# Kernel optimization log

Measured on AMD Instinct MI355X. Metric: run time of the kernel, lower is better.

The kernel has to match this reference:

```python
import jax, jax.numpy as jnp
import numpy as np

B, S, H = 1, 4096, 2048
NH, HD = 16, 128  # num_heads, head_dim = H // NH


def setup_inputs() -> dict:
    key = jax.random.key(0)
    k1, k2, k3 = jax.random.split(key, 3)
    x = jax.random.normal(k1, (B, S, H), dtype=jnp.float32)
    w_qkv = jax.random.normal(k2, (3 * H, H), dtype=jnp.float32) * (1.0 / np.sqrt(H))
    w_out = jax.random.normal(k3, (H, H), dtype=jnp.float32) * (1.0 / np.sqrt(H))
    return {"x": x, "w_qkv": w_qkv, "w_out": w_out}


def reference(x, w_qkv, w_out):
    b, s, _ = x.shape
    # qkv projection: torch Linear computes x @ W^T
    qkv = jnp.einsum('bsh,oh->bso', x, w_qkv)
    qkv = qkv.reshape(b, s, 3, NH, HD).transpose(2, 0, 3, 1, 4)  # [3,B,NH,S,HD]
    q, k, v = qkv[0], qkv[1], qkv[2]
    # world_size == 1 -> single ring step == full attention with online softmax
    scores = jnp.einsum('bhqd,bhkd->bhqk', q, k) / np.sqrt(HD)
    m = jnp.max(scores, axis=-1, keepdims=True)          # running max (single step)
    p = jnp.exp(scores - m)                              # scores_exp
    out = jnp.einsum('bhqk,bhkd->bhqd', p, v)
    denom = jnp.sum(p, axis=-1, keepdims=True) + 1e-8    # running_sum + eps
    out = out / denom
    out = out.transpose(0, 2, 1, 3).reshape(b, s, H)     # [B,S,H]
    return jnp.einsum('bsh,oh->bso', out, w_out)
```

## Files before the change

### kernel.cpp

```cpp
#include <hip/hip_runtime.h>
#include <stdint.h>

typedef __attribute__((ext_vector_type(4))) float f32x4;
typedef __attribute__((ext_vector_type(16))) float f32x16;
typedef __attribute__((ext_vector_type(8))) short bf16x8;
typedef unsigned short u16;

#define MFMA(a, b, c) __builtin_amdgcn_mfma_f32_16x16x32_bf16(a, b, c, 0, 0, 0)
#define MFMA32(a, b, c) __builtin_amdgcn_mfma_f32_32x32x16_bf16(a, b, c, 0, 0, 0)
#define EXP2(x) __builtin_amdgcn_exp2f(x)

__device__ __forceinline__ u16 f2bf(float f) {
  union { float f; unsigned u; } x; x.f = f;
  unsigned r = x.u + 0x7fffu + ((x.u >> 16) & 1u);
  return (u16)(r >> 16);
}

__device__ __forceinline__ unsigned cvtpk(float lo, float hi) {
  unsigned r;
  asm("v_cvt_pk_bf16_f32 %0, %1, %2" : "=v"(r) : "v"(lo), "v"(hi));
  return r;
}

__device__ __forceinline__ void pl32swap(unsigned& a, unsigned& b) {
  asm volatile("v_permlane32_swap_b32 %0, %1" : "+v"(a), "+v"(b));
}

__device__ __forceinline__ void gload16(const void* g, void* l) {
  __builtin_amdgcn_global_load_lds(
      (const __attribute__((address_space(1))) unsigned int*)g,
      (__attribute__((address_space(3))) unsigned int*)l, 16, 0, 0);
}

__global__ void __launch_bounds__(256) cast_bf16(const float* __restrict__ in,
                                                 u16* __restrict__ out, int n4) {
  int i = blockIdx.x * 256 + threadIdx.x;
  if (i >= n4) return;
  float4 v = reinterpret_cast<const float4*>(in)[i];
  ushort4 o;
  o.x = f2bf(v.x); o.y = f2bf(v.y); o.z = f2bf(v.z); o.w = f2bf(v.w);
  reinterpret_cast<ushort4*>(out)[i] = o;
}

template <int EPI>
__global__ void __launch_bounds__(256, 2)
gemm_bt(const u16* __restrict__ A, const u16* __restrict__ B,
        void* __restrict__ C0, void* __restrict__ C1, void* __restrict__ C2,
        int M, int N, int K, int MB) {
  __shared__ alignas(16) u16 sm[8192];
  const int tid = threadIdx.x;
  const int w = tid >> 6, lane = tid & 63;
  const int lr = lane & 15, g = lane >> 4;
  const int gb = (blockIdx.x & 7) * ((int)gridDim.x >> 3) + (blockIdx.x >> 3);
  const int mb = gb % MB, nb = gb / MB;
  const int m0 = mb * 128, n0 = nb * 128;

  const u16* src[4];
  u16* dst[4];
#pragma unroll
  for (int i = 0; i < 4; ++i) {
    int c = w * 4 + i;
    int r = (c & 7) * 16 + (lane >> 2);
    int sb = (lane & 3) ^ ((r >> 1) & 3);
    src[i] = (c < 8) ? (A + (size_t)(m0 + r) * K + sb * 8)
                     : (B + (size_t)(n0 + r) * K + sb * 8);
    dst[i] = &sm[c * 512];
  }

  f32x4 acc[4][4];
#pragma unroll
  for (int x = 0; x < 4; ++x)
#pragma unroll
    for (int y = 0; y < 4; ++y) acc[x][y] = f32x4{0.f, 0.f, 0.f, 0.f};

  const int rowb = (w >> 1) * 64, colb = (w & 1) * 64;
  const int nk = K >> 5;
  for (int kt = 0; kt < nk; ++kt) {
#pragma unroll
    for (int i = 0; i < 4; ++i) gload16(src[i] + kt * 32, dst[i]);
    __syncthreads();
    bf16x8 af[4], bfr[4];
#pragma unroll
    for (int mi = 0; mi < 4; ++mi) {
      int r = rowb + mi * 16 + lr;
      af[mi] = *(const bf16x8*)((const char*)sm + r * 64 +
                                ((g * 16) ^ (((r >> 1) & 3) << 4)));
    }
#pragma unroll
    for (int ni = 0; ni < 4; ++ni) {
      int r = colb + ni * 16 + lr;
      bfr[ni] = *(const bf16x8*)((const char*)sm + 8192 + r * 64 +
                                 ((g * 16) ^ (((r >> 1) & 3) << 4)));
    }
#pragma unroll
    for (int mi = 0; mi < 4; ++mi)
#pragma unroll
      for (int ni = 0; ni < 4; ++ni)
        acc[mi][ni] = MFMA(af[mi], bfr[ni], acc[mi][ni]);
    __syncthreads();
  }

  if (EPI == 0) {
    u16* qo = (u16*)C0;
    u16* ko = (u16*)C1;
    u16* vo = (u16*)C2;
#pragma unroll
    for (int mi = 0; mi < 4; ++mi) {
      int s0 = m0 + rowb + mi * 16 + g * 4;
#pragma unroll
      for (int ni = 0; ni < 4; ++ni) {
        int n = n0 + colb + ni * 16 + lr;
        int t = n >> 11, hh = (n >> 7) & 15, d = n & 127;
        if (t == 2) {
          ushort4 pk;
          pk.x = f2bf(acc[mi][ni][0]);
          pk.y = f2bf(acc[mi][ni][1]);
          pk.z = f2bf(acc[mi][ni][2]);
          pk.w = f2bf(acc[mi][ni][3]);
          *(ushort4*)(vo + (size_t)(hh * 128 + d) * 4096 + s0) = pk;
        } else {
          u16* dq = (t == 0 ? qo : ko) + (size_t)(hh * 4096 + s0) * 128 + d;
#pragma unroll
          for (int j = 0; j < 4; ++j) dq[(size_t)j * 128] = f2bf(acc[mi][ni][j]);
        }
      }
    }
  } else {
    float* C = (float*)C0;
#pragma unroll
    for (int mi = 0; mi < 4; ++mi)
#pragma unroll
      for (int ni = 0; ni < 4; ++ni) {
        size_t r0 = (size_t)(m0 + rowb + mi * 16 + g * 4);
        int cn = n0 + colb + ni * 16 + lr;
#pragma unroll
        for (int j = 0; j < 4; ++j) C[(r0 + j) * N + cn] = acc[mi][ni][j];
      }
  }
}

__global__ void __launch_bounds__(256, 2)
attn_kernel(const u16* __restrict__ qg, const u16* __restrict__ kg,
            const u16* __restrict__ vtg, u16* __restrict__ og) {
  __shared__ alignas(16) u16 sm[32768];
  const int tid = threadIdx.x;
  const int w = tid >> 6, lane = tid & 63;
  const int ql = lane & 31, hl = lane >> 5;
  const int gb = (blockIdx.x & 7) * 64 + (blockIdx.x >> 3);
  const int h = gb >> 5;
  const int qb = gb & 31;

  const u16* ssrc[8];
  u16* sdst[8];
  size_t sstep;
  if (w < 2) {
    sstep = 64 * 128;
#pragma unroll
    for (int i = 0; i < 8; ++i) {
      int c = (w & 1) * 8 + i;
      int r = c * 4 + (lane >> 4);
      int sb = (lane & 15) ^ (r & 7);
      ssrc[i] = kg + (size_t)(h * 4096 + r) * 128 + sb * 8;
      sdst[i] = &sm[c * 512];
    }
  } else {
    sstep = 64;
#pragma unroll
    for (int i = 0; i < 8; ++i) {
      int c = (w & 1) * 8 + i;
      int r = c * 8 + (lane >> 3);
      int sb = (lane & 7) ^ (r & 7);
      ssrc[i] = vtg + (size_t)(h * 128 + r) * 4096 + sb * 8;
      sdst[i] = &sm[16384 + c * 512];
    }
  }

  const u16* qrow = qg + (size_t)(h * 4096 + qb * 128 + w * 32 + ql) * 128 + hl * 8;
  bf16x8 qf[8];
#pragma unroll
  for (int s = 0; s < 8; ++s) qf[s] = *(const bf16x8*)(qrow + s * 16);

  f32x16 of[4];
#pragma unroll
  for (int i = 0; i < 4; ++i)
#pragma unroll
    for (int r = 0; r < 16; ++r) of[i][r] = 0.f;
  float mrun = -1e30f, lsum = 0.f;
  const float sc2 = 0.08838834764831845f * 1.4426950408889634f;
  const float thr = 6.0f / sc2;

#pragma unroll
  for (int i = 0; i < 8; ++i) gload16(ssrc[i], sdst[i]);

  for (int t = 0; t < 64; ++t) {
    const int cur = t & 1;
    asm volatile("s_waitcnt vmcnt(0)" ::: "memory");
    __builtin_amdgcn_s_barrier();
    asm volatile("" ::: "memory");
    if (t + 1 < 64) {
      const int nb = (t + 1) & 1;
#pragma unroll
      for (int i = 0; i < 8; ++i)
        gload16(ssrc[i] + (size_t)(t + 1) * sstep, sdst[i] + nb * 8192);
    }
    const char* kbuf = (const char*)sm + cur * 16384;
    const char* vbuf = (const char*)sm + 32768 + cur * 16384;

    f32x16 st0, st1;
#pragma unroll
    for (int r = 0; r < 16; ++r) { st0[r] = 0.f; st1[r] = 0.f; }
    const int swz = (ql & 7) << 4;
    __builtin_amdgcn_s_setprio(1);
#pragma unroll
    for (int s = 0; s < 8; ++s) {
      int off = (s * 32 + hl * 16) ^ swz;
      bf16x8 k0 = *(const bf16x8*)(kbuf + ql * 256 + off);
      bf16x8 k1 = *(const bf16x8*)(kbuf + (32 + ql) * 256 + off);
      st0 = MFMA32(k0, qf[s], st0);
      st1 = MFMA32(k1, qf[s], st1);
    }
    __builtin_amdgcn_s_setprio(0);

    float tmax = -1e30f;
#pragma unroll
    for (int r = 0; r < 16; ++r) tmax = fmaxf(tmax, fmaxf(st0[r], st1[r]));
    tmax = fmaxf(tmax, __shfl_xor(tmax, 32));
    if (!__all(tmax - mrun <= thr)) {
      float mnew = fmaxf(mrun, tmax);
      float esc = EXP2((mrun - mnew) * sc2);
#pragma unroll
      for (int db = 0; db < 4; ++db)
#pragma unroll
        for (int r = 0; r < 16; ++r) of[db][r] *= esc;
      lsum *= esc;
      mrun = mnew;
    }
    float mb2 = mrun * sc2;
    float psum = 0.f;
    unsigned pk0[8], pk1[8];
#pragma unroll
    for (int i = 0; i < 8; ++i) {
      float a0 = EXP2(st0[2 * i] * sc2 - mb2);
      float b0 = EXP2(st0[2 * i + 1] * sc2 - mb2);
      float a1 = EXP2(st1[2 * i] * sc2 - mb2);
      float b1 = EXP2(st1[2 * i + 1] * sc2 - mb2);
      psum += (a0 + b0) + (a1 + b1);
      pk0[i] = cvtpk(a0, b0);
      pk1[i] = cvtpk(a1, b1);
    }
    psum += __shfl_xor(psum, 32);
    lsum += psum;

    pl32swap(pk0[0], pk0[2]); pl32swap(pk0[1], pk0[3]);
    pl32swap(pk0[4], pk0[6]); pl32swap(pk0[5], pk0[7]);
    pl32swap(pk1[0], pk1[2]); pl32swap(pk1[1], pk1[3]);
    pl32swap(pk1[4], pk1[6]); pl32swap(pk1[5], pk1[7]);
    union U { unsigned u[4]; bf16x8 v; };
    U paf[4];
#pragma unroll
    for (int i = 0; i < 4; ++i) { paf[0].u[i] = pk0[i]; paf[1].u[i] = pk0[4 + i]; }
#pragma unroll
    for (int i = 0; i < 4; ++i) { paf[2].u[i] = pk1[i]; paf[3].u[i] = pk1[4 + i]; }

    __builtin_amdgcn_s_setprio(1);
#pragma unroll
    for (int db = 0; db < 4; ++db) {
      int rr = db * 32 + ql;
      int vswz = (rr & 7) << 4;
#pragma unroll
      for (int kp = 0; kp < 4; ++kp) {
        bf16x8 vf = *(const bf16x8*)(vbuf + rr * 128 + ((kp * 32 + hl * 16) ^ vswz));
        of[db] = MFMA32(vf, paf[kp].v, of[db]);
      }
    }
    __builtin_amdgcn_s_setprio(0);
    asm volatile("" ::: "memory");
  }

  float linv = 1.f / (lsum + 1e-8f);
  size_t qrow_o = (size_t)(qb * 128 + w * 32 + ql) * 2048 + h * 128;
#pragma unroll
  for (int db = 0; db < 4; ++db)
#pragma unroll
    for (int u = 0; u < 4; ++u) {
      ushort4 pk;
      pk.x = f2bf(of[db][4 * u + 0] * linv);
      pk.y = f2bf(of[db][4 * u + 1] * linv);
      pk.z = f2bf(of[db][4 * u + 2] * linv);
      pk.w = f2bf(of[db][4 * u + 3] * linv);
      *(ushort4*)(og + qrow_o + db * 32 + 8 * u + hl * 4) = pk;
    }
}

extern "C" void kernel_launch(void* const* d_in, const int* in_sizes, int n_in,
                              void* d_out, int out_size, void* d_ws, size_t ws_size,
                              hipStream_t stream) {
  const float* x = (const float*)d_in[0];
  const float* w_qkv = (const float*)d_in[1];
  const float* w_out = (const float*)d_in[2];

  char* ws = (char*)d_ws;
  u16* xb = (u16*)(ws + 0);
  u16* wqkvb = (u16*)(ws + 16777216);
  u16* woutb = (u16*)(ws + 41943040);
  u16* qb = (u16*)(ws + 50331648);
  u16* kb = (u16*)(ws + 67108864);
  u16* vtb = (u16*)(ws + 83886080);
  u16* aob = (u16*)(ws + 100663296);

  cast_bf16<<<8192, 256, 0, stream>>>(x, xb, 2097152);
  cast_bf16<<<12288, 256, 0, stream>>>(w_qkv, wqkvb, 3145728);
  cast_bf16<<<4096, 256, 0, stream>>>(w_out, woutb, 1048576);

  gemm_bt<0><<<32 * 48, 256, 0, stream>>>(xb, wqkvb, qb, kb, vtb, 4096, 6144, 2048, 32);
  attn_kernel<<<512, 256, 0, stream>>>(qb, kb, vtb, aob);
  gemm_bt<1><<<32 * 16, 256, 0, stream>>>(aob, woutb, d_out, nullptr, nullptr, 4096, 2048, 2048, 32);
}
```

Measured before the change: 360.5 us.

## Load V fragments directly from global into registers, stage only K in LDS

The attention kernel stops staging the V^T tile in shared memory. Each wave now loads its V fragments straight from global memory into registers at the start of each iteration, and only K is double-buffered in LDS. This halves LDS usage and drops the LDS reads for V. The K swizzle widens to 16 lanes, and vmcnt waits are tuned to overlap the V loads with the QK^T and softmax phase. The trade-offs are higher register pressure (64 extra VGPRs for V) and redundant global V reads across the four waves, which now rely on the cache. The prefetch also wraps around and issues a useless final K load.

Result: slower. 457.0 us (+26.8%).

```diff
diff --git a/kernel.cpp b/kernel.cpp
--- a/kernel.cpp
+++ b/kernel.cpp
@@ -142,7 +142,7 @@
 __global__ void __launch_bounds__(256, 2)
 attn_kernel(const u16* __restrict__ qg, const u16* __restrict__ kg,
             const u16* __restrict__ vtg, u16* __restrict__ og) {
-  __shared__ alignas(16) u16 sm[32768];
+  __shared__ alignas(16) u16 sm[16384];
   const int tid = threadIdx.x;
   const int w = tid >> 6, lane = tid & 63;
   const int ql = lane & 31, hl = lane >> 5;
@@ -150,30 +150,21 @@
   const int h = gb >> 5;
   const int qb = gb & 31;
 
-  const u16* ssrc[8];
-  u16* sdst[8];
-  size_t sstep;
-  if (w < 2) {
-    sstep = 64 * 128;
-#pragma unroll
-    for (int i = 0; i < 8; ++i) {
-      int c = (w & 1) * 8 + i;
-      int r = c * 4 + (lane >> 4);
-      int sb = (lane & 15) ^ (r & 7);
-      ssrc[i] = kg + (size_t)(h * 4096 + r) * 128 + sb * 8;
-      sdst[i] = &sm[c * 512];
-    }
-  } else {
-    sstep = 64;
-#pragma unroll
-    for (int i = 0; i < 8; ++i) {
-      int c = (w & 1) * 8 + i;
-      int r = c * 8 + (lane >> 3);
-      int sb = (lane & 7) ^ (r & 7);
-      ssrc[i] = vtg + (size_t)(h * 128 + r) * 4096 + sb * 8;
-      sdst[i] = &sm[16384 + c * 512];
-    }
-  }
+  const u16* ssrc[4];
+  u16* sdst[4];
+#pragma unroll
+  for (int i = 0; i < 4; ++i) {
+    int c = w * 4 + i;
+    int r = c * 4 + (lane >> 4);
+    int sb = (lane & 15) ^ (r & 15);
+    ssrc[i] = kg + (size_t)(h * 4096 + r) * 128 + sb * 8;
+    sdst[i] = &sm[c * 512];
+  }
+
+  const u16* vbase[4];
+#pragma unroll
+  for (int db = 0; db < 4; ++db)
+    vbase[db] = vtg + (size_t)(h * 128 + db * 32 + ql) * 4096 + hl * 8;
 
   const u16* qrow = qg + (size_t)(h * 4096 + qb * 128 + w * 32 + ql) * 128 + hl * 8;
   bf16x8 qf[8];
@@ -190,30 +181,38 @@
   const float thr = 6.0f / sc2;
 
 #pragma unroll
-  for (int i = 0; i < 8; ++i) gload16(ssrc[i], sdst[i]);
-
+  for (int i = 0; i < 4; ++i) gload16(ssrc[i], sdst[i]);
+
+  const int kxor = (ql & 15) << 4;
   for (int t = 0; t < 64; ++t) {
     const int cur = t & 1;
-    asm volatile("s_waitcnt vmcnt(0)" ::: "memory");
+
+    bf16x8 vfr[4][4];
+#pragma unroll
+    for (int db = 0; db < 4; ++db)
+#pragma unroll
+      for (int kp = 0; kp < 4; ++kp)
+        vfr[db][kp] = *(const bf16x8*)(vbase[db] + t * 64 + kp * 16);
+
+    asm volatile("s_waitcnt vmcnt(16)" ::: "memory");
     __builtin_amdgcn_s_barrier();
-    asm volatile("" ::: "memory");
-    if (t + 1 < 64) {
-      const int nb = (t + 1) & 1;
-#pragma unroll
-      for (int i = 0; i < 8; ++i)
-        gload16(ssrc[i] + (size_t)(t + 1) * sstep, sdst[i] + nb * 8192);
+
+    {
+      const int tn = (t + 1) & 63;
+      const int nb = cur ^ 1;
+#pragma unroll
+      for (int i = 0; i < 4; ++i)
+        gload16(ssrc[i] + (size_t)tn * 8192, sdst[i] + nb * 8192);
     }
     const char* kbuf = (const char*)sm + cur * 16384;
-    const char* vbuf = (const char*)sm + 32768 + cur * 16384;
 
     f32x16 st0, st1;
 #pragma unroll
     for (int r = 0; r < 16; ++r) { st0[r] = 0.f; st1[r] = 0.f; }
-    const int swz = (ql & 7) << 4;
     __builtin_amdgcn_s_setprio(1);
 #pragma unroll
     for (int s = 0; s < 8; ++s) {
-      int off = (s * 32 + hl * 16) ^ swz;
+      int off = ((s * 2 + hl) << 4) ^ kxor;
       bf16x8 k0 = *(const bf16x8*)(kbuf + ql * 256 + off);
       bf16x8 k1 = *(const bf16x8*)(kbuf + (32 + ql) * 256 + off);
       st0 = MFMA32(k0, qf[s], st0);
@@ -262,19 +261,15 @@
 #pragma unroll
     for (int i = 0; i < 4; ++i) { paf[2].u[i] = pk1[i]; paf[3].u[i] = pk1[4 + i]; }
 
+    asm volatile("s_waitcnt vmcnt(4)" ::: "memory");
+
     __builtin_amdgcn_s_setprio(1);
 #pragma unroll
-    for (int db = 0; db < 4; ++db) {
-      int rr = db * 32 + ql;
-      int vswz = (rr & 7) << 4;
-#pragma unroll
-      for (int kp = 0; kp < 4; ++kp) {
-        bf16x8 vf = *(const bf16x8*)(vbuf + rr * 128 + ((kp * 32 + hl * 16) ^ vswz));
-        of[db] = MFMA32(vf, paf[kp].v, of[db]);
-      }
-    }
+    for (int db = 0; db < 4; ++db)
+#pragma unroll
+      for (int kp = 0; kp < 4; ++kp)
+        of[db] = MFMA32(vfr[db][kp], paf[kp].v, of[db]);
     __builtin_amdgcn_s_setprio(0);
-    asm volatile("" ::: "memory");
   }
 
   float linv = 1.f / (lsum + 1e-8f);
```

## Fold softmax scale into Q projection and widen LDS swizzle for K/V tiles

Applied to the files above, without the earlier changes.

The QKV projection epilogue now multiplies Q by the softmax scale times log2(e) before converting to bf16. This lets the attention loop compute exp2(s - m) directly and drops a multiply per score element. The K and V shared-memory layouts switch to a 16-way XOR swizzle, with V pairing two rows per 256-byte line, to reduce LDS bank conflicts on the MFMA operand reads. Pre-scaling Q before rounding to bf16 slightly changes numerics, and the new swizzle index math must match between the global-load and LDS-read sides.

New measurement: 356.8 us. Within noise of the previous version (-1.0%).

```diff
diff --git a/kernel.cpp b/kernel.cpp
--- a/kernel.cpp
+++ b/kernel.cpp
@@ -101,6 +101,7 @@
   }
 
   if (EPI == 0) {
+    const float qs = 0.08838834764831845f * 1.4426950408889634f;
     u16* qo = (u16*)C0;
     u16* ko = (u16*)C1;
     u16* vo = (u16*)C2;
@@ -119,9 +120,10 @@
           pk.w = f2bf(acc[mi][ni][3]);
           *(ushort4*)(vo + (size_t)(hh * 128 + d) * 4096 + s0) = pk;
         } else {
+          float sc = (t == 0) ? qs : 1.f;
           u16* dq = (t == 0 ? qo : ko) + (size_t)(hh * 4096 + s0) * 128 + d;
 #pragma unroll
-          for (int j = 0; j < 4; ++j) dq[(size_t)j * 128] = f2bf(acc[mi][ni][j]);
+          for (int j = 0; j < 4; ++j) dq[(size_t)j * 128] = f2bf(acc[mi][ni][j] * sc);
         }
       }
     }
@@ -159,7 +161,7 @@
     for (int i = 0; i < 8; ++i) {
       int c = (w & 1) * 8 + i;
       int r = c * 4 + (lane >> 4);
-      int sb = (lane & 15) ^ (r & 7);
+      int sb = (lane & 15) ^ (r & 15);
       ssrc[i] = kg + (size_t)(h * 4096 + r) * 128 + sb * 8;
       sdst[i] = &sm[c * 512];
     }
@@ -168,9 +170,10 @@
 #pragma unroll
     for (int i = 0; i < 8; ++i) {
       int c = (w & 1) * 8 + i;
-      int r = c * 8 + (lane >> 3);
-      int sb = (lane & 7) ^ (r & 7);
-      ssrc[i] = vtg + (size_t)(h * 128 + r) * 4096 + sb * 8;
+      int j = c * 4 + (lane >> 4);
+      int x = (lane & 15) ^ (j & 15);
+      int e = x >> 3, b = x & 7;
+      ssrc[i] = vtg + (size_t)(h * 128 + 2 * j + e) * 4096 + b * 8;
       sdst[i] = &sm[16384 + c * 512];
     }
   }
@@ -186,12 +189,13 @@
 #pragma unroll
     for (int r = 0; r < 16; ++r) of[i][r] = 0.f;
   float mrun = -1e30f, lsum = 0.f;
-  const float sc2 = 0.08838834764831845f * 1.4426950408889634f;
-  const float thr = 6.0f / sc2;
+  const float thr = 6.0f;
 
 #pragma unroll
   for (int i = 0; i < 8; ++i) gload16(ssrc[i], sdst[i]);
 
+  const int kxor = (ql & 15) << 4;
+  const int ve8 = (ql & 1) << 3, vxor = ql >> 1;
   for (int t = 0; t < 64; ++t) {
     const int cur = t & 1;
     asm volatile("s_waitcnt vmcnt(0)" ::: "memory");
@@ -209,11 +213,10 @@
     f32x16 st0, st1;
 #pragma unroll
     for (int r = 0; r < 16; ++r) { st0[r] = 0.f; st1[r] = 0.f; }
-    const int swz = (ql & 7) << 4;
     __builtin_amdgcn_s_setprio(1);
 #pragma unroll
     for (int s = 0; s < 8; ++s) {
-      int off = (s * 32 + hl * 16) ^ swz;
+      int off = ((s * 2 + hl) << 4) ^ kxor;
       bf16x8 k0 = *(const bf16x8*)(kbuf + ql * 256 + off);
       bf16x8 k1 = *(const bf16x8*)(kbuf + (32 + ql) * 256 + off);
       st0 = MFMA32(k0, qf[s], st0);
@@ -227,7 +230,7 @@
     tmax = fmaxf(tmax, __shfl_xor(tmax, 32));
     if (!__all(tmax - mrun <= thr)) {
       float mnew = fmaxf(mrun, tmax);
-      float esc = EXP2((mrun - mnew) * sc2);
+      float esc = EXP2(mrun - mnew);
 #pragma unroll
       for (int db = 0; db < 4; ++db)
 #pragma unroll
@@ -235,15 +238,14 @@
       lsum *= esc;
       mrun = mnew;
     }
-    float mb2 = mrun * sc2;
     float psum = 0.f;
     unsigned pk0[8], pk1[8];
 #pragma unroll
     for (int i = 0; i < 8; ++i) {
-      float a0 = EXP2(st0[2 * i] * sc2 - mb2);
-      float b0 = EXP2(st0[2 * i + 1] * sc2 - mb2);
-      float a1 = EXP2(st1[2 * i] * sc2 - mb2);
-      float b1 = EXP2(st1[2 * i + 1] * sc2 - mb2);
+      float a0 = EXP2(st0[2 * i] - mrun);
+      float b0 = EXP2(st0[2 * i + 1] - mrun);
+      float a1 = EXP2(st1[2 * i] - mrun);
+      float b1 = EXP2(st1[2 * i + 1] - mrun);
       psum += (a0 + b0) + (a1 + b1);
       pk0[i] = cvtpk(a0, b0);
       pk1[i] = cvtpk(a1, b1);
@@ -265,11 +267,11 @@
     __builtin_amdgcn_s_setprio(1);
 #pragma unroll
     for (int db = 0; db < 4; ++db) {
-      int rr = db * 32 + ql;
-      int vswz = (rr & 7) << 4;
+      const char* vrow = vbuf + (db * 16 + vxor) * 256;
 #pragma unroll
       for (int kp = 0; kp < 4; ++kp) {
-        bf16x8 vf = *(const bf16x8*)(vbuf + rr * 128 + ((kp * 32 + hl * 16) ^ vswz));
+        int m = (ve8 | (kp * 2 + hl)) ^ vxor;
+        bf16x8 vf = *(const bf16x8*)(vrow + m * 16);
         of[db] = MFMA32(vf, paf[kp].v, of[db]);
       }
     }
```
